# Kernel tuning notes

Measured on AMD Instinct MI355X. Metric: run time of the kernel, lower is better.

Reference implementation:

```python
import jax, jax.numpy as jnp
import numpy as np

N = 50000      # nodes
E = 800000     # edges (before self loops)
H = 4          # heads
C_IN = 128     # input feature dim
C_HID = 64     # per-head out channels (hidden_dim == output_dim)
SLOPE = 0.2    # GATConv leaky_relu negative slope


def setup_inputs() -> dict:
    key = jax.random.key(0)
    ks = jax.random.split(key, 16)
    x = jax.random.normal(ks[0], (N, C_IN), jnp.float32)
    edge_index = jax.random.randint(ks[1], (2, E), 0, N, jnp.int32)

    def p(k, shape):
        return jax.random.normal(k, shape, jnp.float32) * 0.05

    inp = {"x": x, "edge_index": edge_index}
    in_dims = [C_IN, C_HID, C_HID]
    for i in range(3):
        inp[f"W{i+1}"] = p(ks[2 + 4 * i], (in_dims[i], H * C_HID))
        inp[f"asrc{i+1}"] = p(ks[3 + 4 * i], (H, C_HID))
        inp[f"adst{i+1}"] = p(ks[4 + 4 * i], (H, C_HID))
        inp[f"b{i+1}"] = jnp.zeros((C_HID,), jnp.float32)
    return inp


def _gat_layer(x, src, dst, W, a_s, a_d, b):
    # x: [N, F_in]; src/dst: [E'] (self loops included)
    n = x.shape[0]
    h = (x @ W).reshape(n, H, -1)                      # [N, H, C]
    alpha_src = jnp.einsum('nhc,hc->nh', h, a_s)       # att_src . h  (source side)
    alpha_dst = jnp.einsum('nhc,hc->nh', h, a_d)       # att_dst . h  (target side)
    e = jax.nn.leaky_relu(alpha_src[src] + alpha_dst[dst], SLOPE)  # [E', H]
    # scatter-softmax over incoming edges of each dst node
    m = jax.ops.segment_max(e, dst, num_segments=n)    # [N, H]
    ex = jnp.exp(e - m[dst])
    denom = jax.ops.segment_sum(ex, dst, num_segments=n)
    alpha = ex / (denom[dst] + 1e-16)                  # [E', H]
    # scatter-add aggregation of weighted source features
    out = jax.ops.segment_sum(alpha[:, :, None] * h[src], dst, num_segments=n)  # [N, H, C]
    return out.mean(axis=1) + b                        # concat=False -> head mean, + bias


def reference(x, edge_index, W1, asrc1, adst1, b1, W2, asrc2, adst2, b2,
              W3, asrc3, adst3, b3):
    n = x.shape[0]
    loops = jnp.arange(n, dtype=edge_index.dtype)      # GATConv add_self_loops=True
    src = jnp.concatenate([edge_index[0], loops])
    dst = jnp.concatenate([edge_index[1], loops])
    for W, a_s, a_d, b in ((W1, asrc1, adst1, b1),
                           (W2, asrc2, adst2, b2),
                           (W3, asrc3, adst3, b3)):
        x = jax.nn.relu(_gat_layer(x, src, dst, W, a_s, a_d, b))
    return x
```

## Files before the change

kernel.cpp:

```cpp
#include <hip/hip_runtime.h>
#include <hip/hip_bf16.h>
#include <cstddef>

#define NH 4
#define CHID 64
#define HC 256

typedef __attribute__((ext_vector_type(8))) short bf16x8;
typedef __attribute__((ext_vector_type(4))) float f32x4;


__global__ void hist_kernel(const int* __restrict__ ei, int E, int N,
                            int* __restrict__ deg) {
  int i = blockIdx.x * blockDim.x + threadIdx.x;
  int EP = E + N;
  if (i >= EP) return;
  int d = (i < E) ? ei[E + i] : (i - E);
  atomicAdd(&deg[d], 1);
}


__global__ __launch_bounds__(256) void partial_sum_kernel(const int* __restrict__ deg,
                                                          int* __restrict__ part, int n) {
  __shared__ int red[4];
  int t = threadIdx.x;
  int i = blockIdx.x * 256 + t;
  int v = (i < n) ? deg[i] : 0;
#pragma unroll
  for (int o = 32; o; o >>= 1) v += __shfl_xor(v, o, 64);
  if ((t & 63) == 0) red[t >> 6] = v;
  __syncthreads();
  if (t == 0) part[blockIdx.x] = red[0] + red[1] + red[2] + red[3];
}

__global__ __launch_bounds__(256) void scan_part_kernel(int* __restrict__ part, int nb,
                                                        int* __restrict__ row_off, int n) {
  __shared__ int s[256];
  int t = threadIdx.x;
  int v = (t < nb) ? part[t] : 0;
  s[t] = v;
  __syncthreads();
  for (int o = 1; o < 256; o <<= 1) {
    int u = (t >= o) ? s[t - o] : 0;
    __syncthreads();
    s[t] += u;
    __syncthreads();
  }
  if (t < nb) part[t] = s[t] - v;
  if (t == 255) row_off[n] = s[255];
}

__global__ __launch_bounds__(256) void row_off_kernel(const int* __restrict__ deg,
                                                      const int* __restrict__ part,
                                                      int* __restrict__ row_off, int n) {
  __shared__ int s[256];
  int t = threadIdx.x;
  int i = blockIdx.x * 256 + t;
  int v = (i < n) ? deg[i] : 0;
  s[t] = v;
  __syncthreads();
  for (int o = 1; o < 256; o <<= 1) {
    int u = (t >= o) ? s[t - o] : 0;
    __syncthreads();
    s[t] += u;
    __syncthreads();
  }
  if (i < n) row_off[i] = part[blockIdx.x] + s[t] - v;
}

__global__ void scatter_kernel(const int* __restrict__ ei, int E, int N,
                               const int* __restrict__ row_off,
                               int* __restrict__ cursor, int* __restrict__ ssrc) {
  int i = blockIdx.x * blockDim.x + threadIdx.x;
  int EP = E + N;
  if (i >= EP) return;
  int s, d;
  if (i < E) { s = ei[i]; d = ei[E + i]; } else { s = i - E; d = s; }
  int pos = row_off[d] + atomicAdd(&cursor[d], 1);
  ssrc[pos] = s;
}


__global__ void split_x_kernel(const float* __restrict__ x,
                               __hip_bfloat16* __restrict__ hi,
                               __hip_bfloat16* __restrict__ lo, int n4) {
  int i = blockIdx.x * blockDim.x + threadIdx.x;
  if (i >= n4) return;
  float4 v = reinterpret_cast<const float4*>(x)[i];
  __hip_bfloat16 h[4], l[4];
  float f[4] = {v.x, v.y, v.z, v.w};
#pragma unroll
  for (int j = 0; j < 4; ++j) {
    h[j] = __float2bfloat16(f[j]);
    l[j] = __float2bfloat16(f[j] - __bfloat162float(h[j]));
  }
  reinterpret_cast<uint2*>(hi)[i] = *reinterpret_cast<uint2*>(h);
  reinterpret_cast<uint2*>(lo)[i] = *reinterpret_cast<uint2*>(l);
}

__global__ void split_wt3_kernel(const float* __restrict__ W1, const float* __restrict__ W2,
                                 const float* __restrict__ W3,
                                 __hip_bfloat16* __restrict__ w1hi, __hip_bfloat16* __restrict__ w1lo,
                                 __hip_bfloat16* __restrict__ w2hi, __hip_bfloat16* __restrict__ w2lo,
                                 __hip_bfloat16* __restrict__ w3hi, __hip_bfloat16* __restrict__ w3lo) {
  int i = blockIdx.x * blockDim.x + threadIdx.x;
  const float* W; __hip_bfloat16 *hi, *lo; int K, base;
  if (i < 32768)      { W = W1; hi = w1hi; lo = w1lo; K = 128; base = i; }
  else if (i < 49152) { W = W2; hi = w2hi; lo = w2lo; K = 64;  base = i - 32768; }
  else                { W = W3; hi = w3hi; lo = w3lo; K = 64;  base = i - 49152; }
  int k = base >> 8;
  int c = base & 255;
  float v = W[base];
  __hip_bfloat16 h = __float2bfloat16(v);
  hi[c * K + k] = h;
  lo[c * K + k] = __float2bfloat16(v - __bfloat162float(h));
}


__global__ __launch_bounds__(256) void gemm_mfma_kernel(
    const __hip_bfloat16* __restrict__ Ahi, const __hip_bfloat16* __restrict__ Alo,
    const __hip_bfloat16* __restrict__ Bthi, const __hip_bfloat16* __restrict__ Btlo,
    const float* __restrict__ a_s, const float* __restrict__ a_d,
    __hip_bfloat16* __restrict__ h, float* __restrict__ asrc_n,
    float* __restrict__ adst_n, int n_rows, int K, int row_groups) {
  extern __shared__ char smem[];
  uint4* lds4 = reinterpret_cast<uint4*>(smem);
  const int S16 = (256 * K * 2) >> 4;
  const int rowshift = (K == 128) ? 4 : 3;

  {
    const uint4* g_hi = reinterpret_cast<const uint4*>(Bthi);
    const uint4* g_lo = reinterpret_cast<const uint4*>(Btlo);
    for (int c = threadIdx.x; c < S16; c += 256) {
      int row = c >> rowshift;
      int sc = c ^ (row & 7);
      lds4[sc] = g_hi[c];
      lds4[S16 + sc] = g_lo[c];
    }
  }
  __syncthreads();

  int wave = threadIdx.x >> 6;
  int lane = threadIdx.x & 63;
  int n16  = lane & 15;
  int g4   = lane >> 4;
  const bf16x8 z8 = {0, 0, 0, 0, 0, 0, 0, 0};

  for (int g = blockIdx.x; g < row_groups; g += gridDim.x) {
    int row0 = g * 64 + wave * 16;
    int xrow = row0 + n16;
    bool aval = xrow < n_rows;
    size_t xbase = (size_t)xrow * K + g4 * 8;

    f32x4 acc[16];
#pragma unroll
    for (int ct = 0; ct < 16; ++ct) acc[ct] = (f32x4){0.f, 0.f, 0.f, 0.f};

    for (int k0 = 0; k0 < K; k0 += 32) {
      bf16x8 xh = aval ? *reinterpret_cast<const bf16x8*>(&Ahi[xbase + k0]) : z8;
      bf16x8 xl = aval ? *reinterpret_cast<const bf16x8*>(&Alo[xbase + k0]) : z8;
#pragma unroll
      for (int ct = 0; ct < 16; ++ct) {
        int wrow = ct * 16 + n16;
        int ci = ((wrow * K + k0 + g4 * 8) >> 3) ^ (wrow & 7);
        bf16x8 wh = *reinterpret_cast<const bf16x8*>(&lds4[ci]);
        bf16x8 wl = *reinterpret_cast<const bf16x8*>(&lds4[S16 + ci]);
        acc[ct] = __builtin_amdgcn_mfma_f32_16x16x32_bf16(wh, xh, acc[ct], 0, 0, 0);
        acc[ct] = __builtin_amdgcn_mfma_f32_16x16x32_bf16(wh, xl, acc[ct], 0, 0, 0);
        acc[ct] = __builtin_amdgcn_mfma_f32_16x16x32_bf16(wl, xh, acc[ct], 0, 0, 0);
      }
    }

    int r = row0 + n16;
    bool valid = r < n_rows;

    if (valid) {
#pragma unroll
      for (int ct = 0; ct < 16; ++ct) {
        unsigned short u[4];
#pragma unroll
        for (int i = 0; i < 4; ++i) {
          __hip_bfloat16 b = __float2bfloat16(acc[ct][i]);
          u[i] = *reinterpret_cast<unsigned short*>(&b);
        }
        *reinterpret_cast<uint2*>(&h[(size_t)r * HC + ct * 16 + g4 * 4]) =
            *reinterpret_cast<uint2*>(u);
      }
    }

    float ps[NH] = {0.f, 0.f, 0.f, 0.f};
    float pd[NH] = {0.f, 0.f, 0.f, 0.f};
#pragma unroll
    for (int ct = 0; ct < 16; ++ct) {
      int hh = ct >> 2;
      float4 as4 = *reinterpret_cast<const float4*>(&a_s[ct * 16 + g4 * 4]);
      float4 ad4 = *reinterpret_cast<const float4*>(&a_d[ct * 16 + g4 * 4]);
      ps[hh] += acc[ct][0] * as4.x + acc[ct][1] * as4.y + acc[ct][2] * as4.z + acc[ct][3] * as4.w;
      pd[hh] += acc[ct][0] * ad4.x + acc[ct][1] * ad4.y + acc[ct][2] * ad4.z + acc[ct][3] * ad4.w;
    }
#pragma unroll
    for (int hh = 0; hh < NH; ++hh) {
      ps[hh] += __shfl_xor(ps[hh], 16, 64);
      ps[hh] += __shfl_xor(ps[hh], 32, 64);
      pd[hh] += __shfl_xor(pd[hh], 16, 64);
      pd[hh] += __shfl_xor(pd[hh], 32, 64);
    }
    if (lane < 16 && valid) {
      *reinterpret_cast<float4*>(&asrc_n[(size_t)r * NH]) =
          make_float4(ps[0], ps[1], ps[2], ps[3]);
      *reinterpret_cast<float4*>(&adst_n[(size_t)r * NH]) =
          make_float4(pd[0], pd[1], pd[2], pd[3]);
    }
  }
}


__global__ __launch_bounds__(256) void aggregate_kernel(
    const int* __restrict__ row_off, const int* __restrict__ ssrc,
    const __hip_bfloat16* __restrict__ h, const float* __restrict__ asrc_n,
    const float* __restrict__ adst_n, const float* __restrict__ bias,
    __hip_bfloat16* __restrict__ out_hi, __hip_bfloat16* __restrict__ out_lo,
    float* __restrict__ out_f32, int n_nodes) {
  int n = (blockIdx.x * blockDim.x + threadIdx.x) >> 6;
  if (n >= n_nodes) return;
  int l    = threadIdx.x & 63;
  int h2   = l >> 5;
  int lh   = l & 31;
  int head = lh >> 3;
  int beg = row_off[n];
  int deg = row_off[n + 1] - beg;
  float adn = adst_n[n * NH + head];

  float facc[8];
#pragma unroll
  for (int u = 0; u < 8; ++u) facc[u] = 0.f;
  float dsum = 0.f;

  int j = h2;
  int   s0 = 0; float a0 = 0.f; uint4 d0 = {0, 0, 0, 0};
  if (j < deg) {
    s0 = ssrc[beg + j];
    a0 = asrc_n[s0 * NH + head];
    d0 = *reinterpret_cast<const uint4*>(&h[(size_t)s0 * HC + lh * 8]);
  }
  while (j < deg) {
    int jn = j + 2;
    int s1 = 0; float a1 = 0.f; uint4 d1 = {0, 0, 0, 0};
    if (jn < deg) {
      s1 = ssrc[beg + jn];
      a1 = asrc_n[s1 * NH + head];
      d1 = *reinterpret_cast<const uint4*>(&h[(size_t)s1 * HC + lh * 8]);
    }
    float e = a0 + adn;
    e = (e > 0.f) ? e : 0.2f * e;
    float w = __expf(e);
    dsum += w;
    facc[0] += w * __uint_as_float(d0.x << 16);
    facc[1] += w * __uint_as_float(d0.x & 0xffff0000u);
    facc[2] += w * __uint_as_float(d0.y << 16);
    facc[3] += w * __uint_as_float(d0.y & 0xffff0000u);
    facc[4] += w * __uint_as_float(d0.z << 16);
    facc[5] += w * __uint_as_float(d0.z & 0xffff0000u);
    facc[6] += w * __uint_as_float(d0.w << 16);
    facc[7] += w * __uint_as_float(d0.w & 0xffff0000u);
    s0 = s1; a0 = a1; d0 = d1; j = jn;
  }

  dsum += __shfl_xor(dsum, 32, 64);
#pragma unroll
  for (int u = 0; u < 8; ++u) facc[u] += __shfl_xor(facc[u], 32, 64);

  float inv = 1.f / (dsum + 1e-16f);
#pragma unroll
  for (int u = 0; u < 8; ++u) {
    facc[u] *= inv;
    facc[u] += __shfl_xor(facc[u], 8, 64);
    facc[u] += __shfl_xor(facc[u], 16, 64);
  }

  if (l < 8) {
    if (out_f32) {
      float o[8];
#pragma unroll
      for (int u = 0; u < 8; ++u)
        o[u] = fmaxf(0.25f * facc[u] + bias[l * 8 + u], 0.f);
      float4* dst = reinterpret_cast<float4*>(&out_f32[(size_t)n * CHID + l * 8]);
      dst[0] = *reinterpret_cast<float4*>(&o[0]);
      dst[1] = *reinterpret_cast<float4*>(&o[4]);
    } else {
      unsigned short hi8[8], lo8[8];
#pragma unroll
      for (int u = 0; u < 8; ++u) {
        float v = fmaxf(0.25f * facc[u] + bias[l * 8 + u], 0.f);
        __hip_bfloat16 bh = __float2bfloat16(v);
        hi8[u] = *reinterpret_cast<unsigned short*>(&bh);
        __hip_bfloat16 bl = __float2bfloat16(v - __bfloat162float(bh));
        lo8[u] = *reinterpret_cast<unsigned short*>(&bl);
      }
      *reinterpret_cast<uint4*>(&out_hi[(size_t)n * CHID + l * 8]) = *reinterpret_cast<uint4*>(hi8);
      *reinterpret_cast<uint4*>(&out_lo[(size_t)n * CHID + l * 8]) = *reinterpret_cast<uint4*>(lo8);
    }
  }
}


extern "C" void kernel_launch(void* const* d_in, const int* in_sizes, int n_in,
                              void* d_out, int out_size, void* d_ws, size_t ws_size,
                              hipStream_t stream) {
  const float* x   = (const float*)d_in[0];
  const int*   ei  = (const int*)d_in[1];
  const float* W1  = (const float*)d_in[2];
  const float* as1 = (const float*)d_in[3];
  const float* ad1 = (const float*)d_in[4];
  const float* b1  = (const float*)d_in[5];
  const float* W2  = (const float*)d_in[6];
  const float* as2 = (const float*)d_in[7];
  const float* ad2 = (const float*)d_in[8];
  const float* b2  = (const float*)d_in[9];
  const float* W3  = (const float*)d_in[10];
  const float* as3 = (const float*)d_in[11];
  const float* ad3 = (const float*)d_in[12];
  const float* b3  = (const float*)d_in[13];

  int N  = in_sizes[0] / 128;
  int E  = in_sizes[1] / 2;
  int EP = E + N;
  int NB = (N + 255) / 256;

  __hip_bfloat16* h     = (__hip_bfloat16*)d_ws;
  __hip_bfloat16* x1hi  = h + (size_t)N * HC;
  __hip_bfloat16* x1lo  = x1hi + (size_t)N * 128;
  __hip_bfloat16* xhi   = x1lo + (size_t)N * 128;
  __hip_bfloat16* xlo   = xhi + (size_t)N * CHID;
  __hip_bfloat16* w1hi  = xlo + (size_t)N * CHID;
  __hip_bfloat16* w1lo  = w1hi + 256 * 128;
  __hip_bfloat16* w2hi  = w1lo + 256 * 128;
  __hip_bfloat16* w2lo  = w2hi + 256 * 64;
  __hip_bfloat16* w3hi  = w2lo + 256 * 64;
  __hip_bfloat16* w3lo  = w3hi + 256 * 64;
  float* asrc_n = (float*)(w3lo + 256 * 64);
  float* adst_n = asrc_n + (size_t)N * NH;
  int*   deg    = (int*)(adst_n + (size_t)N * NH);
  int*   cursor = deg + N;
  int*   row_off= cursor + N;
  int*   part   = row_off + (N + 1);
  int*   ssrc   = part + ((NB + 3) & ~3);

  hipMemsetAsync(deg, 0, sizeof(int) * (size_t)2 * N, stream);
  int eb = (EP + 255) / 256;
  hist_kernel<<<eb, 256, 0, stream>>>(ei, E, N, deg);
  partial_sum_kernel<<<NB, 256, 0, stream>>>(deg, part, N);
  scan_part_kernel<<<1, 256, 0, stream>>>(part, NB, row_off, N);
  row_off_kernel<<<NB, 256, 0, stream>>>(deg, part, row_off, N);
  scatter_kernel<<<eb, 256, 0, stream>>>(ei, E, N, row_off, cursor, ssrc);

  split_x_kernel<<<(N * 128 / 4 + 255) / 256, 256, 0, stream>>>(x, x1hi, x1lo, N * 128 / 4);
  split_wt3_kernel<<<(65536 + 255) / 256, 256, 0, stream>>>(W1, W2, W3, w1hi, w1lo,
                                                            w2hi, w2lo, w3hi, w3lo);

  (void)hipFuncSetAttribute(reinterpret_cast<const void*>(gemm_mfma_kernel),
                            hipFuncAttributeMaxDynamicSharedMemorySize, 131072);

  int RG = (N + 63) / 64;
  int ablocks = (N + 3) / 4;

  gemm_mfma_kernel<<<256, 256, 131072, stream>>>(x1hi, x1lo, w1hi, w1lo, as1, ad1,
                                                 h, asrc_n, adst_n, N, 128, RG);
  aggregate_kernel<<<ablocks, 256, 0, stream>>>(row_off, ssrc, h, asrc_n, adst_n, b1,
                                                xhi, xlo, nullptr, N);
  gemm_mfma_kernel<<<512, 256, 65536, stream>>>(xhi, xlo, w2hi, w2lo, as2, ad2,
                                                h, asrc_n, adst_n, N, 64, RG);
  aggregate_kernel<<<ablocks, 256, 0, stream>>>(row_off, ssrc, h, asrc_n, adst_n, b2,
                                                xhi, xlo, nullptr, N);
  gemm_mfma_kernel<<<512, 256, 65536, stream>>>(xhi, xlo, w3hi, w3lo, as3, ad3,
                                                h, asrc_n, adst_n, N, 64, RG);
  aggregate_kernel<<<ablocks, 256, 0, stream>>>(row_off, ssrc, h, asrc_n, adst_n, b3,
                                                nullptr, nullptr, (float*)d_out, N);
}
```

Before: 400.1 us.

## Precompute edge softmax weights, drop weight lo split, restructure aggregation

The weight matrices are no longer split into hi/lo bf16 parts, so the GEMM issues two MFMAs per tile instead of three and stages half as much LDS. A new per-edge kernel computes exp(leaky_relu) weights for all four heads, using a stored dst array from the CSR scatter. Aggregation now has each lane handle 8 edges across all heads with double-buffered loads, instead of two edges per head group. GEMM grids now launch one block per row group. The trade is extra edge-weight buffer traffic, an added launch per layer, and slightly lower GEMM precision.

Measured after the change: 409.8 us. 1.02x slower.

```diff
diff --git a/kernel.cpp b/kernel.cpp
--- a/kernel.cpp
+++ b/kernel.cpp
@@ -18,7 +18,6 @@
   int d = (i < E) ? ei[E + i] : (i - E);
   atomicAdd(&deg[d], 1);
 }
-
 
 __global__ __launch_bounds__(256) void partial_sum_kernel(const int* __restrict__ deg,
                                                           int* __restrict__ part, int n) {
@@ -70,7 +69,8 @@
 
 __global__ void scatter_kernel(const int* __restrict__ ei, int E, int N,
                                const int* __restrict__ row_off,
-                               int* __restrict__ cursor, int* __restrict__ ssrc) {
+                               int* __restrict__ cursor, int* __restrict__ ssrc,
+                               int* __restrict__ sdst) {
   int i = blockIdx.x * blockDim.x + threadIdx.x;
   int EP = E + N;
   if (i >= EP) return;
@@ -78,6 +78,7 @@
   if (i < E) { s = ei[i]; d = ei[E + i]; } else { s = i - E; d = s; }
   int pos = row_off[d] + atomicAdd(&cursor[d], 1);
   ssrc[pos] = s;
+  sdst[pos] = d;
 }
 
 
@@ -100,26 +101,23 @@
 
 __global__ void split_wt3_kernel(const float* __restrict__ W1, const float* __restrict__ W2,
                                  const float* __restrict__ W3,
-                                 __hip_bfloat16* __restrict__ w1hi, __hip_bfloat16* __restrict__ w1lo,
-                                 __hip_bfloat16* __restrict__ w2hi, __hip_bfloat16* __restrict__ w2lo,
-                                 __hip_bfloat16* __restrict__ w3hi, __hip_bfloat16* __restrict__ w3lo) {
+                                 __hip_bfloat16* __restrict__ w1hi,
+                                 __hip_bfloat16* __restrict__ w2hi,
+                                 __hip_bfloat16* __restrict__ w3hi) {
   int i = blockIdx.x * blockDim.x + threadIdx.x;
-  const float* W; __hip_bfloat16 *hi, *lo; int K, base;
-  if (i < 32768)      { W = W1; hi = w1hi; lo = w1lo; K = 128; base = i; }
-  else if (i < 49152) { W = W2; hi = w2hi; lo = w2lo; K = 64;  base = i - 32768; }
-  else                { W = W3; hi = w3hi; lo = w3lo; K = 64;  base = i - 49152; }
+  const float* W; __hip_bfloat16* hi; int K, base;
+  if (i < 32768)      { W = W1; hi = w1hi; K = 128; base = i; }
+  else if (i < 49152) { W = W2; hi = w2hi; K = 64;  base = i - 32768; }
+  else                { W = W3; hi = w3hi; K = 64;  base = i - 49152; }
   int k = base >> 8;
   int c = base & 255;
-  float v = W[base];
-  __hip_bfloat16 h = __float2bfloat16(v);
-  hi[c * K + k] = h;
-  lo[c * K + k] = __float2bfloat16(v - __bfloat162float(h));
+  hi[c * K + k] = __float2bfloat16(W[base]);
 }
 
 
 __global__ __launch_bounds__(256) void gemm_mfma_kernel(
     const __hip_bfloat16* __restrict__ Ahi, const __hip_bfloat16* __restrict__ Alo,
-    const __hip_bfloat16* __restrict__ Bthi, const __hip_bfloat16* __restrict__ Btlo,
+    const __hip_bfloat16* __restrict__ Bthi,
     const float* __restrict__ a_s, const float* __restrict__ a_d,
     __hip_bfloat16* __restrict__ h, float* __restrict__ asrc_n,
     float* __restrict__ adst_n, int n_rows, int K, int row_groups) {
@@ -130,12 +128,9 @@
 
   {
     const uint4* g_hi = reinterpret_cast<const uint4*>(Bthi);
-    const uint4* g_lo = reinterpret_cast<const uint4*>(Btlo);
     for (int c = threadIdx.x; c < S16; c += 256) {
       int row = c >> rowshift;
-      int sc = c ^ (row & 7);
-      lds4[sc] = g_hi[c];
-      lds4[S16 + sc] = g_lo[c];
+      lds4[c ^ (row & 7)] = g_hi[c];
     }
   }
   __syncthreads();
@@ -164,10 +159,8 @@
         int wrow = ct * 16 + n16;
         int ci = ((wrow * K + k0 + g4 * 8) >> 3) ^ (wrow & 7);
         bf16x8 wh = *reinterpret_cast<const bf16x8*>(&lds4[ci]);
-        bf16x8 wl = *reinterpret_cast<const bf16x8*>(&lds4[S16 + ci]);
         acc[ct] = __builtin_amdgcn_mfma_f32_16x16x32_bf16(wh, xh, acc[ct], 0, 0, 0);
         acc[ct] = __builtin_amdgcn_mfma_f32_16x16x32_bf16(wh, xl, acc[ct], 0, 0, 0);
-        acc[ct] = __builtin_amdgcn_mfma_f32_16x16x32_bf16(wl, xh, acc[ct], 0, 0, 0);
       }
     }
 
@@ -215,90 +208,143 @@
 }
 
 
+__global__ void edge_weight_kernel(const int* __restrict__ ssrc, const int* __restrict__ sdst,
+                                   const float* __restrict__ asrc_n,
+                                   const float* __restrict__ adst_n,
+                                   float4* __restrict__ wbuf, int EP) {
+  int i = blockIdx.x * blockDim.x + threadIdx.x;
+  if (i >= EP) return;
+  int s = ssrc[i];
+  int d = sdst[i];
+  float4 a = reinterpret_cast<const float4*>(asrc_n)[s];
+  float4 b = reinterpret_cast<const float4*>(adst_n)[d];
+  float e0 = a.x + b.x; e0 = (e0 > 0.f) ? e0 : 0.2f * e0;
+  float e1 = a.y + b.y; e1 = (e1 > 0.f) ? e1 : 0.2f * e1;
+  float e2 = a.z + b.z; e2 = (e2 > 0.f) ? e2 : 0.2f * e2;
+  float e3 = a.w + b.w; e3 = (e3 > 0.f) ? e3 : 0.2f * e3;
+  wbuf[i] = make_float4(__expf(e0), __expf(e1), __expf(e2), __expf(e3));
+}
+
+
 __global__ __launch_bounds__(256) void aggregate_kernel(
     const int* __restrict__ row_off, const int* __restrict__ ssrc,
-    const __hip_bfloat16* __restrict__ h, const float* __restrict__ asrc_n,
-    const float* __restrict__ adst_n, const float* __restrict__ bias,
+    const __hip_bfloat16* __restrict__ h, const float4* __restrict__ wbuf,
+    const float* __restrict__ bias,
     __hip_bfloat16* __restrict__ out_hi, __hip_bfloat16* __restrict__ out_lo,
     float* __restrict__ out_f32, int n_nodes) {
   int n = (blockIdx.x * blockDim.x + threadIdx.x) >> 6;
   if (n >= n_nodes) return;
   int l    = threadIdx.x & 63;
-  int h2   = l >> 5;
-  int lh   = l & 31;
-  int head = lh >> 3;
-  int beg = row_off[n];
-  int deg = row_off[n + 1] - beg;
-  float adn = adst_n[n * NH + head];
-
-  float facc[8];
-#pragma unroll
-  for (int u = 0; u < 8; ++u) facc[u] = 0.f;
-  float dsum = 0.f;
-
-  int j = h2;
-  int   s0 = 0; float a0 = 0.f; uint4 d0 = {0, 0, 0, 0};
-  if (j < deg) {
-    s0 = ssrc[beg + j];
-    a0 = asrc_n[s0 * NH + head];
-    d0 = *reinterpret_cast<const uint4*>(&h[(size_t)s0 * HC + lh * 8]);
-  }
-  while (j < deg) {
-    int jn = j + 2;
-    int s1 = 0; float a1 = 0.f; uint4 d1 = {0, 0, 0, 0};
-    if (jn < deg) {
-      s1 = ssrc[beg + jn];
-      a1 = asrc_n[s1 * NH + head];
-      d1 = *reinterpret_cast<const uint4*>(&h[(size_t)s1 * HC + lh * 8]);
-    }
-    float e = a0 + adn;
-    e = (e > 0.f) ? e : 0.2f * e;
-    float w = __expf(e);
-    dsum += w;
-    facc[0] += w * __uint_as_float(d0.x << 16);
-    facc[1] += w * __uint_as_float(d0.x & 0xffff0000u);
-    facc[2] += w * __uint_as_float(d0.y << 16);
-    facc[3] += w * __uint_as_float(d0.y & 0xffff0000u);
-    facc[4] += w * __uint_as_float(d0.z << 16);
-    facc[5] += w * __uint_as_float(d0.z & 0xffff0000u);
-    facc[6] += w * __uint_as_float(d0.w << 16);
-    facc[7] += w * __uint_as_float(d0.w & 0xffff0000u);
-    s0 = s1; a0 = a1; d0 = d1; j = jn;
-  }
-
-  dsum += __shfl_xor(dsum, 32, 64);
-#pragma unroll
-  for (int u = 0; u < 8; ++u) facc[u] += __shfl_xor(facc[u], 32, 64);
-
-  float inv = 1.f / (dsum + 1e-16f);
+  int slot = l >> 3;
+  int cp   = l & 7;
+  int beg  = row_off[n];
+  int deg  = row_off[n + 1] - beg;
+
+  float facc[32];
+#pragma unroll
+  for (int u = 0; u < 32; ++u) facc[u] = 0.f;
+  float4 ds = make_float4(0.f, 0.f, 0.f, 0.f);
+  const float4 z4 = make_float4(0.f, 0.f, 0.f, 0.f);
+  const uint4 zu = {0, 0, 0, 0};
+
+  const char* hbase = reinterpret_cast<const char*>(h);
+
+  auto LOADE = [&](int j, float4& w4, uint4* d) {
+    int jj  = j + slot;
+    int idx = beg + min(jj, deg - 1);
+    int sv  = ssrc[idx];
+    float4 w = wbuf[idx];
+    bool ok = jj < deg;
+    w4.x = ok ? w.x : 0.f;
+    w4.y = ok ? w.y : 0.f;
+    w4.z = ok ? w.z : 0.f;
+    w4.w = ok ? w.w : 0.f;
+    const char* hp = hbase + (size_t)sv * 512 + cp * 16;
+    d[0] = *reinterpret_cast<const uint4*>(hp);
+    d[1] = *reinterpret_cast<const uint4*>(hp + 128);
+    d[2] = *reinterpret_cast<const uint4*>(hp + 256);
+    d[3] = *reinterpret_cast<const uint4*>(hp + 384);
+  };
+
+  auto PROC = [&](const float4& w4, const uint4* d) {
+    ds.x += w4.x; ds.y += w4.y; ds.z += w4.z; ds.w += w4.w;
+#pragma unroll
+    for (int hh = 0; hh < 4; ++hh) {
+      float w = (hh == 0) ? w4.x : (hh == 1) ? w4.y : (hh == 2) ? w4.z : w4.w;
+      uint4 dd = d[hh];
+      facc[hh * 8 + 0] += w * __uint_as_float(dd.x << 16);
+      facc[hh * 8 + 1] += w * __uint_as_float(dd.x & 0xffff0000u);
+      facc[hh * 8 + 2] += w * __uint_as_float(dd.y << 16);
+      facc[hh * 8 + 3] += w * __uint_as_float(dd.y & 0xffff0000u);
+      facc[hh * 8 + 4] += w * __uint_as_float(dd.z << 16);
+      facc[hh * 8 + 5] += w * __uint_as_float(dd.z & 0xffff0000u);
+      facc[hh * 8 + 6] += w * __uint_as_float(dd.w << 16);
+      facc[hh * 8 + 7] += w * __uint_as_float(dd.w & 0xffff0000u);
+    }
+  };
+
+  float4 wA = z4, wB = z4;
+  uint4 dA[4] = {zu, zu, zu, zu};
+  uint4 dB[4] = {zu, zu, zu, zu};
+
+  LOADE(0, wA, dA);
+  for (int j = 0; j < deg; j += 16) {
+    if (j + 8 < deg) LOADE(j + 8, wB, dB); else wB = z4;
+    PROC(wA, dA);
+    if (j + 16 < deg) LOADE(j + 16, wA, dA); else wA = z4;
+    PROC(wB, dB);
+  }
+
+#pragma unroll
+  for (int o = 8; o <= 32; o <<= 1) {
+    ds.x += __shfl_xor(ds.x, o, 64);
+    ds.y += __shfl_xor(ds.y, o, 64);
+    ds.z += __shfl_xor(ds.z, o, 64);
+    ds.w += __shfl_xor(ds.w, o, 64);
+  }
+  float iv0 = 1.f / (ds.x + 1e-16f);
+  float iv1 = 1.f / (ds.y + 1e-16f);
+  float iv2 = 1.f / (ds.z + 1e-16f);
+  float iv3 = 1.f / (ds.w + 1e-16f);
+
+  float v[8];
+#pragma unroll
+  for (int u = 0; u < 8; ++u)
+    v[u] = facc[u] * iv0 + facc[8 + u] * iv1 + facc[16 + u] * iv2 + facc[24 + u] * iv3;
+
 #pragma unroll
   for (int u = 0; u < 8; ++u) {
-    facc[u] *= inv;
-    facc[u] += __shfl_xor(facc[u], 8, 64);
-    facc[u] += __shfl_xor(facc[u], 16, 64);
-  }
-
-  if (l < 8) {
+    v[u] += __shfl_xor(v[u], 8, 64);
+    v[u] += __shfl_xor(v[u], 16, 64);
+    v[u] += __shfl_xor(v[u], 32, 64);
+  }
+
+  if (slot < 2) {
+    float o0 = (slot == 0) ? v[0] : v[4];
+    float o1 = (slot == 0) ? v[1] : v[5];
+    float o2 = (slot == 0) ? v[2] : v[6];
+    float o3 = (slot == 0) ? v[3] : v[7];
+    int ch = cp * 8 + slot * 4;
+    float4 b4 = *reinterpret_cast<const float4*>(&bias[ch]);
+    o0 = fmaxf(0.25f * o0 + b4.x, 0.f);
+    o1 = fmaxf(0.25f * o1 + b4.y, 0.f);
+    o2 = fmaxf(0.25f * o2 + b4.z, 0.f);
+    o3 = fmaxf(0.25f * o3 + b4.w, 0.f);
     if (out_f32) {
-      float o[8];
-#pragma unroll
-      for (int u = 0; u < 8; ++u)
-        o[u] = fmaxf(0.25f * facc[u] + bias[l * 8 + u], 0.f);
-      float4* dst = reinterpret_cast<float4*>(&out_f32[(size_t)n * CHID + l * 8]);
-      dst[0] = *reinterpret_cast<float4*>(&o[0]);
-      dst[1] = *reinterpret_cast<float4*>(&o[4]);
+      *reinterpret_cast<float4*>(&out_f32[(size_t)n * CHID + ch]) =
+          make_float4(o0, o1, o2, o3);
     } else {
-      unsigned short hi8[8], lo8[8];
-#pragma unroll
-      for (int u = 0; u < 8; ++u) {
-        float v = fmaxf(0.25f * facc[u] + bias[l * 8 + u], 0.f);
-        __hip_bfloat16 bh = __float2bfloat16(v);
-        hi8[u] = *reinterpret_cast<unsigned short*>(&bh);
-        __hip_bfloat16 bl = __float2bfloat16(v - __bfloat162float(bh));
-        lo8[u] = *reinterpret_cast<unsigned short*>(&bl);
+      float of[4] = {o0, o1, o2, o3};
+      unsigned short hi4[4], lo4[4];
+#pragma unroll
+      for (int u = 0; u < 4; ++u) {
+        __hip_bfloat16 bh = __float2bfloat16(of[u]);
+        hi4[u] = *reinterpret_cast<unsigned short*>(&bh);
+        __hip_bfloat16 bl = __float2bfloat16(of[u] - __bfloat162float(bh));
+        lo4[u] = *reinterpret_cast<unsigned short*>(&bl);
       }
-      *reinterpret_cast<uint4*>(&out_hi[(size_t)n * CHID + l * 8]) = *reinterpret_cast<uint4*>(hi8);
-      *reinterpret_cast<uint4*>(&out_lo[(size_t)n * CHID + l * 8]) = *reinterpret_cast<uint4*>(lo8);
+      *reinterpret_cast<uint2*>(&out_hi[(size_t)n * CHID + ch]) = *reinterpret_cast<uint2*>(hi4);
+      *reinterpret_cast<uint2*>(&out_lo[(size_t)n * CHID + ch]) = *reinterpret_cast<uint2*>(lo4);
     }
   }
 }
@@ -333,18 +379,17 @@
   __hip_bfloat16* xhi   = x1lo + (size_t)N * 128;
   __hip_bfloat16* xlo   = xhi + (size_t)N * CHID;
   __hip_bfloat16* w1hi  = xlo + (size_t)N * CHID;
-  __hip_bfloat16* w1lo  = w1hi + 256 * 128;
-  __hip_bfloat16* w2hi  = w1lo + 256 * 128;
-  __hip_bfloat16* w2lo  = w2hi + 256 * 64;
-  __hip_bfloat16* w3hi  = w2lo + 256 * 64;
-  __hip_bfloat16* w3lo  = w3hi + 256 * 64;
-  float* asrc_n = (float*)(w3lo + 256 * 64);
+  __hip_bfloat16* w2hi  = w1hi + 256 * 128;
+  __hip_bfloat16* w3hi  = w2hi + 256 * 64;
+  float* asrc_n = (float*)(w3hi + 256 * 64);
   float* adst_n = asrc_n + (size_t)N * NH;
-  int*   deg    = (int*)(adst_n + (size_t)N * NH);
+  float4* wbuf  = (float4*)(adst_n + (size_t)N * NH);
+  int*   deg    = (int*)(wbuf + EP);
   int*   cursor = deg + N;
   int*   row_off= cursor + N;
   int*   part   = row_off + (N + 1);
   int*   ssrc   = part + ((NB + 3) & ~3);
+  int*   sdst   = ssrc + EP;
 
   hipMemsetAsync(deg, 0, sizeof(int) * (size_t)2 * N, stream);
   int eb = (EP + 255) / 256;
@@ -352,11 +397,10 @@
   partial_sum_kernel<<<NB, 256, 0, stream>>>(deg, part, N);
   scan_part_kernel<<<1, 256, 0, stream>>>(part, NB, row_off, N);
   row_off_kernel<<<NB, 256, 0, stream>>>(deg, part, row_off, N);
-  scatter_kernel<<<eb, 256, 0, stream>>>(ei, E, N, row_off, cursor, ssrc);
+  scatter_kernel<<<eb, 256, 0, stream>>>(ei, E, N, row_off, cursor, ssrc, sdst);
 
   split_x_kernel<<<(N * 128 / 4 + 255) / 256, 256, 0, stream>>>(x, x1hi, x1lo, N * 128 / 4);
-  split_wt3_kernel<<<(65536 + 255) / 256, 256, 0, stream>>>(W1, W2, W3, w1hi, w1lo,
-                                                            w2hi, w2lo, w3hi, w3lo);
+  split_wt3_kernel<<<(65536 + 255) / 256, 256, 0, stream>>>(W1, W2, W3, w1hi, w2hi, w3hi);
 
   (void)hipFuncSetAttribute(reinterpret_cast<const void*>(gemm_mfma_kernel),
                             hipFuncAttributeMaxDynamicSharedMemorySize, 131072);
@@ -364,16 +408,19 @@
   int RG = (N + 63) / 64;
   int ablocks = (N + 3) / 4;
 
-  gemm_mfma_kernel<<<256, 256, 131072, stream>>>(x1hi, x1lo, w1hi, w1lo, as1, ad1,
-                                                 h, asrc_n, adst_n, N, 128, RG);
-  aggregate_kernel<<<ablocks, 256, 0, stream>>>(row_off, ssrc, h, asrc_n, adst_n, b1,
+  gemm_mfma_kernel<<<RG, 256, 65536, stream>>>(x1hi, x1lo, w1hi, as1, ad1,
+                                               h, asrc_n, adst_n, N, 128, RG);
+  edge_weight_kernel<<<eb, 256, 0, stream>>>(ssrc, sdst, asrc_n, adst_n, wbuf, EP);
+  aggregate_kernel<<<ablocks, 256, 0, stream>>>(row_off, ssrc, h, wbuf, b1,
                                                 xhi, xlo, nullptr, N);
-  gemm_mfma_kernel<<<512, 256, 65536, stream>>>(xhi, xlo, w2hi, w2lo, as2, ad2,
-                                                h, asrc_n, adst_n, N, 64, RG);
-  aggregate_kernel<<<ablocks, 256, 0, stream>>>(row_off, ssrc, h, asrc_n, adst_n, b2,
+  gemm_mfma_kernel<<<RG, 256, 32768, stream>>>(xhi, xlo, w2hi, as2, ad2,
+                                               h, asrc_n, adst_n, N, 64, RG);
+  edge_weight_kernel<<<eb, 256, 0, stream>>>(ssrc, sdst, asrc_n, adst_n, wbuf, EP);
+  aggregate_kernel<<<ablocks, 256, 0, stream>>>(row_off, ssrc, h, wbuf, b2,
                                                 xhi, xlo, nullptr, N);
-  gemm_mfma_kernel<<<512, 256, 65536, stream>>>(xhi, xlo, w3hi, w3lo, as3, ad3,
-                                                h, asrc_n, adst_n, N, 64, RG);
-  aggregate_kernel<<<ablocks, 256, 0, stream>>>(row_off, ssrc, h, asrc_n, adst_n, b3,
+  gemm_mfma_kernel<<<RG, 256, 32768, stream>>>(xhi, xlo, w3hi, as3, ad3,
+                                               h, asrc_n, adst_n, N, 64, RG);
+  edge_weight_kernel<<<eb, 256, 0, stream>>>(ssrc, sdst, asrc_n, adst_n, wbuf, EP);
+  aggregate_kernel<<<ablocks, 256, 0, stream>>>(row_off, ssrc, h, wbuf, b3,
                                                 nullptr, nullptr, (float*)d_out, N);
 }
```
